# Optimization experiments

Hardware: AMD Instinct MI355X
Metric: run time of the kernel (lower is better)

## Reference

```python
import jax, jax.numpy as jnp
import numpy as np

L = 880      # flattened RootMLP param count: (1*8+8) + (8*96+96)
HID = 8      # MLP hidden width
OUT = 96     # 2*data_size
DS = 48      # data_size
T = 64       # sequence length
BATCH = 4


def setup_inputs() -> dict:
    key = jax.random.key(0)
    k1, k2, k3, k4, k5 = jax.random.split(key, 5)
    xs = jax.random.normal(k1, (BATCH, T, DS), jnp.float32)
    ts = jax.random.uniform(k2, (BATCH, T), dtype=jnp.float32)
    theta0 = 0.1 * jax.random.normal(k3, (L,), jnp.float32)
    # near-identity A so matrix powers up to A^(T-1) stay bounded
    A = 0.99 * jnp.eye(L, dtype=jnp.float32) + (0.01 / np.sqrt(L)) * jax.random.normal(k4, (L, L), jnp.float32)
    B = 0.01 * jax.random.normal(k5, (L, DS), jnp.float32)
    return {"xs": xs, "ts": ts, "theta0": theta0, "A": A, "B": B, "aux": 0}


def _forward(xs, ts, theta0, A, B):
    Bt, T_, _ = xs.shape
    I = jnp.eye(L, dtype=A.dtype)

    # A_pows[t] = A^t for t = 0..T-1, via a cumulative matmul scan
    def step(P, _):
        return P @ A, P
    _, pows = jax.lax.scan(step, I, None, length=T_)  # (T, L, L)

    # K_conv = [B, A^0(A-I)B, ..., A^(T-3)(A-I)B]  -> (T-1, L, DS)
    M = (A - I) @ B
    K_tail = jnp.einsum('tij,jd->tid', pows[:T_ - 2], M)
    K_conv = jnp.concatenate([B[None], K_tail], axis=0)

    # FFT circular convolution of input signal with K_conv over time
    u = xs[:, 1:, :]                      # (B, T-1, DS)
    u_f = jnp.fft.fft(u, axis=1)
    K_f = jnp.fft.fft(K_conv, axis=0)     # (T-1, L, DS)
    thetas = jnp.fft.ifft(jnp.einsum('tld,btd->btl', K_f, u_f), axis=1).real

    # initial-condition convolution with K_conv0 = A^tau, tau = 0..T-2
    K0 = pows[:T_ - 1]                    # (T-1, L, L)
    sig = jnp.zeros((Bt, T_ - 1, L), xs.dtype)
    sig = sig.at[:, 0, :].set(theta0)
    sig = sig.at[:, 1, :].set(-(xs[:, 0, :] @ B.T))
    sig_f = jnp.fft.fft(sig, axis=1)
    K0_f = jnp.fft.fft(K0, axis=0)
    phi0 = jnp.fft.ifft(jnp.einsum('tlm,btm->btl', K0_f, sig_f), axis=1).real

    thetas = thetas + phi0
    thetas = jnp.concatenate([jnp.broadcast_to(theta0, (Bt, 1, L)), thetas], axis=1)  # (B, T, L)

    # apply RootMLP (1 -> HID -> OUT) with params unflattened from thetas
    W0 = thetas[..., :HID]                                    # (B,T,HID): W0 is (HID,1)
    b0 = thetas[..., HID:2 * HID]
    W1 = thetas[..., 2 * HID:2 * HID + OUT * HID].reshape(Bt, T_, OUT, HID)
    b1 = thetas[..., 2 * HID + OUT * HID:]
    h = jax.nn.relu(W0 * ts[..., None] + b0)                  # (B,T,HID)
    out = jnp.einsum('btoh,bth->bto', W1, h) + b1             # (B,T,OUT)
    # reconstruction head: tanh means, softplus stds
    return jnp.concatenate([jnp.tanh(out[..., :DS]), jax.nn.softplus(out[..., DS:])], axis=-1)


def reference(xs, ts, theta0, A, B, aux):
    return _forward(xs, ts, theta0, A, B)
```

## Files before the change

### kernel.cpp

```cpp
#include <hip/hip_runtime.h>
#include <math.h>

typedef unsigned int uint;
typedef unsigned short ushort;
typedef short s16x8 __attribute__((ext_vector_type(8)));
typedef float f32x4 __attribute__((ext_vector_type(4)));
typedef uint u32x4 __attribute__((ext_vector_type(4)));

#define L     880
#define LP    896
#define NC    64
#define WS    (NC * LP)
#define DS    48
#define OUTD  96
#define KCV   3072
#define NZ    3

#define OFF_E    0
#define OFF_WF   4415488
#define OFF_WB   (OFF_WF + 63 * WS)
#define OFF_KDT  (OFF_WB + 63 * WS / 2)
#define OFF_U    (OFF_KDT + LP * KCV / 2)
#define OFF_PART (OFF_U + 256 * KCV / 2)

__device__ inline ushort f2b(float f) {
  uint u = __builtin_bit_cast(uint, f);
  u += 0x7fffu + ((u >> 16) & 1u);
  return (ushort)(u >> 16);
}
__device__ inline float b2f(ushort b) {
  uint u = ((uint)b) << 16;
  return __builtin_bit_cast(float, u);
}

__global__ __launch_bounds__(256) void k_prepE(const float* __restrict__ A,
                                               ushort* __restrict__ EN,
                                               ushort* __restrict__ ET) {
  __shared__ float T[64][65];
  const int bi = blockIdx.y * 64, bj = blockIdx.x * 64;
  const int tid = threadIdx.x;
  const int r = tid >> 2, c0 = (tid & 3) * 16;
  const int gi = bi + r;
#pragma unroll
  for (int q = 0; q < 4; ++q) {
    int c = c0 + q * 4, gj = bj + c;
    float4 v = {0.f, 0.f, 0.f, 0.f};
    if (gi < L && gj < L) {
      v = *(const float4*)(A + gi * L + gj);
      if (gi == gj)     v.x -= 0.99f;
      if (gi == gj + 1) v.y -= 0.99f;
      if (gi == gj + 2) v.z -= 0.99f;
      if (gi == gj + 3) v.w -= 0.99f;
    }
    T[r][c] = v.x; T[r][c + 1] = v.y; T[r][c + 2] = v.z; T[r][c + 3] = v.w;
  }
  __syncthreads();
  {
    union { ushort s[16]; u32x4 v[2]; } pk;
#pragma unroll
    for (int i = 0; i < 16; ++i) pk.s[i] = f2b(T[r][c0 + i]);
    *(u32x4*)(EN + (size_t)(bi + r) * LP + bj + c0)     = pk.v[0];
    *(u32x4*)(EN + (size_t)(bi + r) * LP + bj + c0 + 8) = pk.v[1];
  }
  {
    union { ushort s[16]; u32x4 v[2]; } pk;
#pragma unroll
    for (int i = 0; i < 16; ++i) pk.s[i] = f2b(T[c0 + i][r]);
    *(u32x4*)(ET + (size_t)(bj + r) * LP + bi + c0)     = pk.v[0];
    *(u32x4*)(ET + (size_t)(bj + r) * LP + bi + c0 + 8) = pk.v[1];
  }
}

__global__ void k_prepW0(const float* __restrict__ B, const float* __restrict__ th0,
                         const float* __restrict__ xs, float* __restrict__ WF,
                         ushort* __restrict__ WB) {
  int idx = blockIdx.x * 256 + threadIdx.x;
  int c = idx / LP, l = idx % LP;
  float v = 0.f;
  if (l < L) {
    if (c < DS) v = B[l * DS + c];
    else if (c == DS) v = th0[l];
    else if (c < 53) {
      int b = c - 49;
      float s = 0.f;
      for (int d = 0; d < DS; ++d) s += B[l * DS + d] * xs[(b * 64) * DS + d];
      v = -s;
    }
  }
  WF[idx] = v;
  WB[idx] = f2b(v);
}

__global__ __launch_bounds__(256) void k_ladder(
    const ushort* __restrict__ sqA, const ushort* __restrict__ sqBT, float cs2,
    ushort* __restrict__ sqOutN, ushort* __restrict__ sqOutT, int ySq,
    const ushort* __restrict__ chA, const ushort* __restrict__ chBT, float csc,
    const float* __restrict__ chWFin, float* __restrict__ chWFout,
    ushort* __restrict__ chWBout) {
  __shared__ __align__(16) ushort As[2][64][72];
  __shared__ __align__(16) ushort Bs[2][64][72];
  const int tid = threadIdx.x;
  const bool isSq = (int)blockIdx.y < ySq;
  const int n0 = blockIdx.x * 64;
  const int m0 = isSq ? blockIdx.y * 64 : ((int)blockIdx.y - ySq) * 64;
  const ushort* Ab = isSq ? sqA : chA;
  const ushort* Bb = isSq ? sqBT : chBT;
  const int r = tid >> 2, kq = (tid & 3) * 16;
  const ushort* aptr = Ab + (size_t)(m0 + r) * LP + kq;
  const ushort* bptr = Bb + (size_t)(n0 + r) * LP + kq;
  const int wv = tid >> 6, lane = tid & 63;
  const int wm = (wv >> 1) * 32, wn = (wv & 1) * 32;
  const int lr = lane & 15, lg = lane >> 4;
  f32x4 acc[2][2] = {};
  u32x4 ra0 = *(const u32x4*)aptr;
  u32x4 ra1 = *(const u32x4*)(aptr + 8);
  u32x4 rb0 = *(const u32x4*)bptr;
  u32x4 rb1 = *(const u32x4*)(bptr + 8);
  const int kI = LP / 64;
  for (int it = 0; it < kI; ++it) {
    const int cur = it & 1;
    *(u32x4*)&As[cur][r][kq]     = ra0;
    *(u32x4*)&As[cur][r][kq + 8] = ra1;
    *(u32x4*)&Bs[cur][r][kq]     = rb0;
    *(u32x4*)&Bs[cur][r][kq + 8] = rb1;
    __syncthreads();
    if (it + 1 < kI) {
      ra0 = *(const u32x4*)(aptr + (it + 1) * 64);
      ra1 = *(const u32x4*)(aptr + (it + 1) * 64 + 8);
      rb0 = *(const u32x4*)(bptr + (it + 1) * 64);
      rb1 = *(const u32x4*)(bptr + (it + 1) * 64 + 8);
    }
#pragma unroll
    for (int ks = 0; ks < 2; ++ks) {
      s16x8 a0 = *(const s16x8*)&As[cur][wm + lr][ks * 32 + lg * 8];
      s16x8 a1 = *(const s16x8*)&As[cur][wm + 16 + lr][ks * 32 + lg * 8];
      s16x8 b0 = *(const s16x8*)&Bs[cur][wn + lr][ks * 32 + lg * 8];
      s16x8 b1 = *(const s16x8*)&Bs[cur][wn + 16 + lr][ks * 32 + lg * 8];
      acc[0][0] = __builtin_amdgcn_mfma_f32_16x16x32_bf16(a0, b0, acc[0][0], 0, 0, 0);
      acc[0][1] = __builtin_amdgcn_mfma_f32_16x16x32_bf16(a0, b1, acc[0][1], 0, 0, 0);
      acc[1][0] = __builtin_amdgcn_mfma_f32_16x16x32_bf16(a1, b0, acc[1][0], 0, 0, 0);
      acc[1][1] = __builtin_amdgcn_mfma_f32_16x16x32_bf16(a1, b1, acc[1][1], 0, 0, 0);
    }
  }
  if (isSq) {
    ushort (*T)[72] = As[0];
    __syncthreads();
#pragma unroll
    for (int fm = 0; fm < 2; ++fm)
#pragma unroll
      for (int fn = 0; fn < 2; ++fn)
#pragma unroll
        for (int rr = 0; rr < 4; ++rr) {
          int mi = wm + fm * 16 + lg * 4 + rr;
          int ni = wn + fn * 16 + lr;
          float v = acc[fm][fn][rr] + cs2 * b2f(sqA[(size_t)(m0 + mi) * LP + n0 + ni]);
          ushort bv = f2b(v);
          sqOutN[(size_t)(m0 + mi) * LP + n0 + ni] = bv;
          T[ni][mi] = bv;
        }
    if (sqOutT) {
      __syncthreads();
      int rt = tid >> 2, ct0 = (tid & 3) * 16;
      u32x4 o0 = *(const u32x4*)&T[rt][ct0];
      u32x4 o1 = *(const u32x4*)&T[rt][ct0 + 8];
      *(u32x4*)(sqOutT + (size_t)(n0 + rt) * LP + m0 + ct0)     = o0;
      *(u32x4*)(sqOutT + (size_t)(n0 + rt) * LP + m0 + ct0 + 8) = o1;
    }
  } else {
#pragma unroll
    for (int fm = 0; fm < 2; ++fm)
#pragma unroll
      for (int fn = 0; fn < 2; ++fn)
#pragma unroll
        for (int rr = 0; rr < 4; ++rr) {
          int m = m0 + wm + fm * 16 + lg * 4 + rr;
          int n = n0 + wn + fn * 16 + lr;
          float v = acc[fm][fn][rr] + csc * chWFin[(size_t)m * LP + n];
          chWFout[(size_t)m * LP + n] = v;
          chWBout[(size_t)m * LP + n] = f2b(v);
        }
  }
}

__global__ void k_kd(const float* __restrict__ WF, ushort* __restrict__ KDT) {
  __shared__ float D[48][65];
  const int j = blockIdx.x;
  const int l0 = blockIdx.y * 64;
  if (j < 63) {
    const float* Wj = WF + (size_t)j * WS;
    for (int e = threadIdx.x; e < 48 * 64; e += 256) {
      int d = e >> 6, ll = e & 63;
      float v = Wj[d * LP + l0 + ll];
      if (j > 0) v -= Wj[-(int)WS + d * LP + l0 + ll];
      D[d][ll] = v;
    }
  } else {
    for (int e = threadIdx.x; e < 48 * 64; e += 256) { int d = e >> 6, ll = e & 63; D[d][ll] = 0.f; }
  }
  __syncthreads();
  for (int e = threadIdx.x; e < 48 * 64; e += 256) {
    int ll = e / 48, d = e - ll * 48;
    KDT[(size_t)(l0 + ll) * KCV + j * 48 + d] = f2b(D[d][ll]);
  }
}

__global__ void k_u(const float* __restrict__ xs, ushort* __restrict__ U) {
  int idx = (blockIdx.x * 256 + threadIdx.x) * 4;
  int rr = idx / KCV, k = idx - rr * KCV;
  ushort4 v = {0, 0, 0, 0};
  if (rr < 252 && k < 3024) {
    int b = rr / 63, tau = rr - b * 63;
    int j = k / DS, d = k - j * DS;
    int s = tau - j; if (s < 0) s += 63;
    float4 x4 = *(const float4*)(xs + (size_t)(b * 64 + s + 1) * DS + d);
    v.x = f2b(x4.x); v.y = f2b(x4.y); v.z = f2b(x4.z); v.w = f2b(x4.w);
  }
  *(ushort4*)(U + idx) = v;
}

__global__ __launch_bounds__(256) void k_conv(const ushort* __restrict__ U,
                                              const ushort* __restrict__ KDT,
                                              float* __restrict__ part) {
  __shared__ __align__(16) ushort As[2][64][72];
  __shared__ __align__(16) ushort Bs[2][64][72];
  const int tid = threadIdx.x;
  const int n0 = blockIdx.x * 64, m0 = blockIdx.y * 64;
  const int kbase = blockIdx.z * (KCV / NZ);
  const int r = tid >> 2, kq = (tid & 3) * 16;
  const ushort* aptr = U + (size_t)(m0 + r) * KCV + kbase + kq;
  const ushort* bptr = KDT + (size_t)(n0 + r) * KCV + kbase + kq;
  const int wv = tid >> 6, lane = tid & 63;
  const int wm = (wv >> 1) * 32, wn = (wv & 1) * 32;
  const int lr = lane & 15, lg = lane >> 4;
  f32x4 acc[2][2] = {};
  u32x4 ra0 = *(const u32x4*)aptr;
  u32x4 ra1 = *(const u32x4*)(aptr + 8);
  u32x4 rb0 = *(const u32x4*)bptr;
  u32x4 rb1 = *(const u32x4*)(bptr + 8);
  const int kI = (KCV / NZ) / 64;
  for (int it = 0; it < kI; ++it) {
    const int cur = it & 1;
    *(u32x4*)&As[cur][r][kq]     = ra0;
    *(u32x4*)&As[cur][r][kq + 8] = ra1;
    *(u32x4*)&Bs[cur][r][kq]     = rb0;
    *(u32x4*)&Bs[cur][r][kq + 8] = rb1;
    __syncthreads();
    if (it + 1 < kI) {
      ra0 = *(const u32x4*)(aptr + (it + 1) * 64);
      ra1 = *(const u32x4*)(aptr + (it + 1) * 64 + 8);
      rb0 = *(const u32x4*)(bptr + (it + 1) * 64);
      rb1 = *(const u32x4*)(bptr + (it + 1) * 64 + 8);
    }
#pragma unroll
    for (int ks = 0; ks < 2; ++ks) {
      s16x8 a0 = *(const s16x8*)&As[cur][wm + lr][ks * 32 + lg * 8];
      s16x8 a1 = *(const s16x8*)&As[cur][wm + 16 + lr][ks * 32 + lg * 8];
      s16x8 b0 = *(const s16x8*)&Bs[cur][wn + lr][ks * 32 + lg * 8];
      s16x8 b1 = *(const s16x8*)&Bs[cur][wn + 16 + lr][ks * 32 + lg * 8];
      acc[0][0] = __builtin_amdgcn_mfma_f32_16x16x32_bf16(a0, b0, acc[0][0], 0, 0, 0);
      acc[0][1] = __builtin_amdgcn_mfma_f32_16x16x32_bf16(a0, b1, acc[0][1], 0, 0, 0);
      acc[1][0] = __builtin_amdgcn_mfma_f32_16x16x32_bf16(a1, b0, acc[1][0], 0, 0, 0);
      acc[1][1] = __builtin_amdgcn_mfma_f32_16x16x32_bf16(a1, b1, acc[1][1], 0, 0, 0);
    }
  }
  float* pp = part + (size_t)blockIdx.z * (256 * LP);
#pragma unroll
  for (int fm = 0; fm < 2; ++fm)
#pragma unroll
    for (int fn = 0; fn < 2; ++fn)
#pragma unroll
      for (int rr = 0; rr < 4; ++rr) {
        int m = m0 + wm + fm * 16 + lg * 4 + rr;
        int n = n0 + wn + fn * 16 + lr;
        pp[(size_t)m * LP + n] = acc[fm][fn][rr];
      }
}

__global__ __launch_bounds__(256) void k_final(const float* __restrict__ part,
                                               const float* __restrict__ WF,
                                               const float* __restrict__ th0,
                                               const float* __restrict__ ts,
                                               float* __restrict__ out) {
  __shared__ float th[LP];
  const int bt = blockIdx.x, b = bt >> 6, t = bt & 63;
  for (int l = threadIdx.x; l < LP; l += 256) {
    float v = 0.f;
    if (l < L) {
      if (t == 0) v = th0[l];
      else {
        int rr = b * 63 + (t - 1);
        v = part[(size_t)rr * LP + l]
          + part[(size_t)(256 * LP) + rr * LP + l]
          + part[(size_t)(2 * 256 * LP) + rr * LP + l];
        int tau = t - 1;
        v += WF[(size_t)tau * WS + DS * LP + l];
        int tw = (tau + 62) % 63;
        v += WF[(size_t)tw * WS + (49 + b) * LP + l];
      }
    }
    th[l] = v;
  }
  __syncthreads();
  int o = threadIdx.x;
  if (o < OUTD) {
    float tv = ts[bt];
    float acc = th[784 + o];
#pragma unroll
    for (int i = 0; i < 8; ++i) {
      float h = fmaxf(th[i] * tv + th[8 + i], 0.f);
      acc += th[16 + o * 8 + i] * h;
    }
    float rs;
    if (o < DS) rs = tanhf(acc);
    else        rs = fmaxf(acc, 0.f) + log1pf(expf(-fabsf(acc)));
    out[bt * OUTD + o] = rs;
  }
}

extern "C" void kernel_launch(void* const* d_in, const int* in_sizes, int n_in,
                              void* d_out, int out_size, void* d_ws, size_t ws_size,
                              hipStream_t stream) {
  const float* xs  = (const float*)d_in[0];
  const float* ts  = (const float*)d_in[1];
  const float* th0 = (const float*)d_in[2];
  const float* A   = (const float*)d_in[3];
  const float* B   = (const float*)d_in[4];
  float* out = (float*)d_out;
  float* ws  = (float*)d_ws;

  ushort* EP   = (ushort*)(ws + OFF_E);
  const size_t PL = (size_t)LP * LP;
  ushort* EN1  = EP + 0 * PL;
  ushort* ET1  = EP + 1 * PL;
  ushort* EN2  = EP + 2 * PL;
  ushort* ET2  = EP + 3 * PL;
  ushort* EN4  = EP + 4 * PL;
  ushort* ET4  = EP + 5 * PL;
  ushort* EN8  = EP + 6 * PL;
  ushort* ET8  = EP + 7 * PL;
  ushort* EN16 = EP + 8 * PL;
  ushort* ET16 = EP + 9 * PL;
  ushort* EN32 = EP + 10 * PL;
  float*  WF   = ws + OFF_WF;
  ushort* WB   = (ushort*)(ws + OFF_WB);
  ushort* KDT  = (ushort*)(ws + OFF_KDT);
  ushort* U    = (ushort*)(ws + OFF_U);
  float*  part = ws + OFF_PART;

  const float c1 = 0.99f;
  const float c2 = c1 * c1, c4 = c2 * c2, c8 = c4 * c4, c16 = c8 * c8, c32 = c16 * c16;

  k_prepE<<<dim3(14, 14), 256, 0, stream>>>(A, EN1, ET1);
  k_prepW0<<<(NC * LP) / 256, 256, 0, stream>>>(B, th0, xs, WF, WB);
  k_u<<<(256 * KCV / 4) / 256, 256, 0, stream>>>(xs, U);

  k_ladder<<<dim3(14, 15), 256, 0, stream>>>(EN1, ET1, 2.f * c1, EN2, ET2, 14,
                                             WB, EN1, c1, WF, WF + 1 * WS, WB + (size_t)1 * WS);
  k_ladder<<<dim3(14, 16), 256, 0, stream>>>(EN2, ET2, 2.f * c2, EN4, ET4, 14,
                                             WB, EN2, c2, WF, WF + 2 * WS, WB + (size_t)2 * WS);
  k_ladder<<<dim3(14, 18), 256, 0, stream>>>(EN4, ET4, 2.f * c4, EN8, ET8, 14,
                                             WB, EN4, c4, WF, WF + 4 * WS, WB + (size_t)4 * WS);
  k_ladder<<<dim3(14, 22), 256, 0, stream>>>(EN8, ET8, 2.f * c8, EN16, ET16, 14,
                                             WB, EN8, c8, WF, WF + 8 * WS, WB + (size_t)8 * WS);
  k_ladder<<<dim3(14, 30), 256, 0, stream>>>(EN16, ET16, 2.f * c16, EN32, nullptr, 14,
                                             WB, EN16, c16, WF, WF + 16 * WS, WB + (size_t)16 * WS);
  k_ladder<<<dim3(14, 31), 256, 0, stream>>>(nullptr, nullptr, 0.f, nullptr, nullptr, 0,
                                             WB, EN32, c32, WF, WF + 32 * WS, WB + (size_t)32 * WS);

  k_kd<<<dim3(64, 14), 256, 0, stream>>>(WF, KDT);
  k_conv<<<dim3(14, 4, NZ), 256, 0, stream>>>(U, KDT, part);
  k_final<<<256, 256, 0, stream>>>(part, WF, th0, ts, out);
}
```

Measured before the change: 110.7 us.

## Enlarge GEMM tiles to 128x64, merge prep kernels, share a GEMM core macro

Three setup kernels (E transpose/convert, W0 init, U Toeplitz build) are merged into one launch that dispatches on block index. The ladder and convolution GEMMs move from 64x64 to 128x64 tiles through a shared macro, so each wave computes 4x2 MFMA fragments, giving more reuse per LDS load and fewer blocks. Chain rows are clamped to a valid-row count with guarded stores, and the WF/WB buffers grow to 64 slots to absorb the larger tiles. The cost is fewer blocks per launch (lower occupancy on a wide GPU) and more registers and LDS per block.

Measured after the change: 157.9 us. +42.6%, slower.

```diff
diff --git a/kernel.cpp b/kernel.cpp
--- a/kernel.cpp
+++ b/kernel.cpp
@@ -18,8 +18,8 @@
 
 #define OFF_E    0
 #define OFF_WF   4415488
-#define OFF_WB   (OFF_WF + 63 * WS)
-#define OFF_KDT  (OFF_WB + 63 * WS / 2)
+#define OFF_WB   (OFF_WF + 64 * WS)
+#define OFF_KDT  (OFF_WB + 64 * WS / 2)
 #define OFF_U    (OFF_KDT + LP * KCV / 2)
 #define OFF_PART (OFF_U + 256 * KCV / 2)
 
@@ -33,120 +33,159 @@
   return __builtin_bit_cast(float, u);
 }
 
-__global__ __launch_bounds__(256) void k_prepE(const float* __restrict__ A,
-                                               ushort* __restrict__ EN,
-                                               ushort* __restrict__ ET) {
-  __shared__ float T[64][65];
-  const int bi = blockIdx.y * 64, bj = blockIdx.x * 64;
+__global__ __launch_bounds__(256) void k_prep(const float* __restrict__ A,
+                                              const float* __restrict__ B,
+                                              const float* __restrict__ th0,
+                                              const float* __restrict__ xs,
+                                              ushort* __restrict__ EN,
+                                              ushort* __restrict__ ET,
+                                              float* __restrict__ WF,
+                                              ushort* __restrict__ WB,
+                                              ushort* __restrict__ U) {
+  const int blk = blockIdx.x;
   const int tid = threadIdx.x;
-  const int r = tid >> 2, c0 = (tid & 3) * 16;
-  const int gi = bi + r;
-#pragma unroll
-  for (int q = 0; q < 4; ++q) {
-    int c = c0 + q * 4, gj = bj + c;
-    float4 v = {0.f, 0.f, 0.f, 0.f};
-    if (gi < L && gj < L) {
-      v = *(const float4*)(A + gi * L + gj);
+  if (blk < 196) {
+    __shared__ float T[64][65];
+    const int bi = (blk / 14) * 64, bj = (blk % 14) * 64;
+    const int r = tid >> 2, c0 = (tid & 3) * 16;
+    const int gi = bi + r;
+#pragma unroll
+    for (int q = 0; q < 4; ++q) {
+      int c = c0 + q * 4, gj = bj + c;
+      float4 v = {0.f, 0.f, 0.f, 0.f};
+      if (gi < L && gj + 3 < L) {
+        v = *(const float4*)(A + (size_t)gi * L + gj);
+      } else if (gi < L) {
+        if (gj + 0 < L) v.x = A[(size_t)gi * L + gj];
+        if (gj + 1 < L) v.y = A[(size_t)gi * L + gj + 1];
+        if (gj + 2 < L) v.z = A[(size_t)gi * L + gj + 2];
+        if (gj + 3 < L) v.w = A[(size_t)gi * L + gj + 3];
+      }
       if (gi == gj)     v.x -= 0.99f;
       if (gi == gj + 1) v.y -= 0.99f;
       if (gi == gj + 2) v.z -= 0.99f;
       if (gi == gj + 3) v.w -= 0.99f;
-    }
-    T[r][c] = v.x; T[r][c + 1] = v.y; T[r][c + 2] = v.z; T[r][c + 3] = v.w;
-  }
-  __syncthreads();
-  {
-    union { ushort s[16]; u32x4 v[2]; } pk;
-#pragma unroll
-    for (int i = 0; i < 16; ++i) pk.s[i] = f2b(T[r][c0 + i]);
-    *(u32x4*)(EN + (size_t)(bi + r) * LP + bj + c0)     = pk.v[0];
-    *(u32x4*)(EN + (size_t)(bi + r) * LP + bj + c0 + 8) = pk.v[1];
-  }
-  {
-    union { ushort s[16]; u32x4 v[2]; } pk;
-#pragma unroll
-    for (int i = 0; i < 16; ++i) pk.s[i] = f2b(T[c0 + i][r]);
-    *(u32x4*)(ET + (size_t)(bj + r) * LP + bi + c0)     = pk.v[0];
-    *(u32x4*)(ET + (size_t)(bj + r) * LP + bi + c0 + 8) = pk.v[1];
-  }
-}
-
-__global__ void k_prepW0(const float* __restrict__ B, const float* __restrict__ th0,
-                         const float* __restrict__ xs, float* __restrict__ WF,
-                         ushort* __restrict__ WB) {
-  int idx = blockIdx.x * 256 + threadIdx.x;
-  int c = idx / LP, l = idx % LP;
-  float v = 0.f;
-  if (l < L) {
-    if (c < DS) v = B[l * DS + c];
-    else if (c == DS) v = th0[l];
-    else if (c < 53) {
-      int b = c - 49;
-      float s = 0.f;
-      for (int d = 0; d < DS; ++d) s += B[l * DS + d] * xs[(b * 64) * DS + d];
-      v = -s;
-    }
-  }
-  WF[idx] = v;
-  WB[idx] = f2b(v);
-}
+      T[r][c] = v.x; T[r][c + 1] = v.y; T[r][c + 2] = v.z; T[r][c + 3] = v.w;
+    }
+    __syncthreads();
+    {
+      union { ushort s[16]; u32x4 v[2]; } pk;
+#pragma unroll
+      for (int i = 0; i < 16; ++i) pk.s[i] = f2b(T[r][c0 + i]);
+      *(u32x4*)(EN + (size_t)(bi + r) * LP + bj + c0)     = pk.v[0];
+      *(u32x4*)(EN + (size_t)(bi + r) * LP + bj + c0 + 8) = pk.v[1];
+    }
+    {
+      union { ushort s[16]; u32x4 v[2]; } pk;
+#pragma unroll
+      for (int i = 0; i < 16; ++i) pk.s[i] = f2b(T[c0 + i][r]);
+      *(u32x4*)(ET + (size_t)(bj + r) * LP + bi + c0)     = pk.v[0];
+      *(u32x4*)(ET + (size_t)(bj + r) * LP + bi + c0 + 8) = pk.v[1];
+    }
+  } else if (blk < 420) {
+    int idx = (blk - 196) * 256 + tid;
+    int c = idx / LP, l = idx % LP;
+    float v = 0.f;
+    if (l < L) {
+      if (c < DS) v = B[l * DS + c];
+      else if (c == DS) v = th0[l];
+      else if (c < 53) {
+        int b = c - 49;
+        float s = 0.f;
+        for (int d = 0; d < DS; ++d) s += B[l * DS + d] * xs[(b * 64) * DS + d];
+        v = -s;
+      }
+    }
+    WF[idx] = v;
+    WB[idx] = f2b(v);
+  } else {
+    int idx = ((blk - 420) * 256 + tid) * 4;
+    int rr = idx / KCV, k = idx - rr * KCV;
+    ushort4 v = {0, 0, 0, 0};
+    if (rr < 252 && k < 3024) {
+      int b = rr / 63, tau = rr - b * 63;
+      int j = k / DS, d = k - j * DS;
+      int s = tau - j; if (s < 0) s += 63;
+      float4 x4 = *(const float4*)(xs + (size_t)(b * 64 + s + 1) * DS + d);
+      v.x = f2b(x4.x); v.y = f2b(x4.y); v.z = f2b(x4.z); v.w = f2b(x4.w);
+    }
+    *(ushort4*)(U + idx) = v;
+  }
+}
+
+#define LAD_ITERS (LP / 64)
+
+#define GEMM_CORE(Aop, BopT, Kdim, kIters, kOff, Mv, m0, n0)                       \
+  const int ar = tid >> 3;                                                         \
+  const int ak = (tid & 7) * 8;                                                    \
+  const int br = tid >> 2;                                                         \
+  const int bk = (tid & 3) * 8;                                                    \
+  const ushort* ap[4];                                                             \
+  _Pragma("unroll")                                                                \
+  for (int i = 0; i < 4; ++i) {                                                    \
+    int rowi = m0 + ar + i * 32;                                                   \
+    if (rowi > Mv - 1) rowi = Mv - 1;                                              \
+    ap[i] = Aop + (size_t)rowi * Kdim + kOff + ak;                                 \
+  }                                                                                \
+  const ushort* bp0 = BopT + (size_t)(n0 + br) * Kdim + kOff + bk;                 \
+  const ushort* bp1 = bp0 + 32;                                                    \
+  const int wv = tid >> 6, lane = tid & 63;                                        \
+  const int wm = (wv >> 1) * 64, wn = (wv & 1) * 32;                               \
+  const int lr = lane & 15, lg = lane >> 4;                                        \
+  f32x4 acc[4][2] = {};                                                            \
+  u32x4 ra[4], rb[2];                                                              \
+  _Pragma("unroll")                                                                \
+  for (int i = 0; i < 4; ++i) ra[i] = *(const u32x4*)ap[i];                        \
+  rb[0] = *(const u32x4*)bp0;                                                      \
+  rb[1] = *(const u32x4*)bp1;                                                      \
+  for (int it = 0; it < kIters; ++it) {                                            \
+    const int cur = it & 1;                                                        \
+    _Pragma("unroll")                                                              \
+    for (int i = 0; i < 4; ++i) *(u32x4*)&As[cur][ar + i * 32][ak] = ra[i];        \
+    *(u32x4*)&Bs[cur][br][bk]      = rb[0];                                        \
+    *(u32x4*)&Bs[cur][br][bk + 32] = rb[1];                                        \
+    __syncthreads();                                                               \
+    if (it + 1 < kIters) {                                                         \
+      _Pragma("unroll")                                                            \
+      for (int i = 0; i < 4; ++i) ra[i] = *(const u32x4*)(ap[i] + (it + 1) * 64);  \
+      rb[0] = *(const u32x4*)(bp0 + (it + 1) * 64);                                \
+      rb[1] = *(const u32x4*)(bp1 + (it + 1) * 64);                                \
+    }                                                                              \
+    _Pragma("unroll")                                                              \
+    for (int k2 = 0; k2 < 2; ++k2) {                                               \
+      s16x8 af[4], bf[2];                                                          \
+      _Pragma("unroll")                                                            \
+      for (int m = 0; m < 4; ++m) af[m] = *(const s16x8*)&As[cur][wm + m * 16 + lr][k2 * 32 + lg * 8]; \
+      _Pragma("unroll")                                                            \
+      for (int n = 0; n < 2; ++n) bf[n] = *(const s16x8*)&Bs[cur][wn + n * 16 + lr][k2 * 32 + lg * 8]; \
+      _Pragma("unroll")                                                            \
+      for (int m = 0; m < 4; ++m)                                                  \
+        _Pragma("unroll")                                                          \
+        for (int n = 0; n < 2; ++n)                                                \
+          acc[m][n] = __builtin_amdgcn_mfma_f32_16x16x32_bf16(af[m], bf[n], acc[m][n], 0, 0, 0); \
+    }                                                                              \
+  }
 
 __global__ __launch_bounds__(256) void k_ladder(
     const ushort* __restrict__ sqA, const ushort* __restrict__ sqBT, float cs2,
     ushort* __restrict__ sqOutN, ushort* __restrict__ sqOutT, int ySq,
     const ushort* __restrict__ chA, const ushort* __restrict__ chBT, float csc,
     const float* __restrict__ chWFin, float* __restrict__ chWFout,
-    ushort* __restrict__ chWBout) {
-  __shared__ __align__(16) ushort As[2][64][72];
+    ushort* __restrict__ chWBout, int Mv) {
+  __shared__ __align__(16) ushort As[2][128][72];
   __shared__ __align__(16) ushort Bs[2][64][72];
   const int tid = threadIdx.x;
   const bool isSq = (int)blockIdx.y < ySq;
   const int n0 = blockIdx.x * 64;
-  const int m0 = isSq ? blockIdx.y * 64 : ((int)blockIdx.y - ySq) * 64;
+  const int m0 = isSq ? blockIdx.y * 128 : ((int)blockIdx.y - ySq) * 128;
+  const int MvEff = isSq ? LP : Mv;
   const ushort* Ab = isSq ? sqA : chA;
   const ushort* Bb = isSq ? sqBT : chBT;
-  const int r = tid >> 2, kq = (tid & 3) * 16;
-  const ushort* aptr = Ab + (size_t)(m0 + r) * LP + kq;
-  const ushort* bptr = Bb + (size_t)(n0 + r) * LP + kq;
-  const int wv = tid >> 6, lane = tid & 63;
-  const int wm = (wv >> 1) * 32, wn = (wv & 1) * 32;
-  const int lr = lane & 15, lg = lane >> 4;
-  f32x4 acc[2][2] = {};
-  u32x4 ra0 = *(const u32x4*)aptr;
-  u32x4 ra1 = *(const u32x4*)(aptr + 8);
-  u32x4 rb0 = *(const u32x4*)bptr;
-  u32x4 rb1 = *(const u32x4*)(bptr + 8);
-  const int kI = LP / 64;
-  for (int it = 0; it < kI; ++it) {
-    const int cur = it & 1;
-    *(u32x4*)&As[cur][r][kq]     = ra0;
-    *(u32x4*)&As[cur][r][kq + 8] = ra1;
-    *(u32x4*)&Bs[cur][r][kq]     = rb0;
-    *(u32x4*)&Bs[cur][r][kq + 8] = rb1;
-    __syncthreads();
-    if (it + 1 < kI) {
-      ra0 = *(const u32x4*)(aptr + (it + 1) * 64);
-      ra1 = *(const u32x4*)(aptr + (it + 1) * 64 + 8);
-      rb0 = *(const u32x4*)(bptr + (it + 1) * 64);
-      rb1 = *(const u32x4*)(bptr + (it + 1) * 64 + 8);
-    }
-#pragma unroll
-    for (int ks = 0; ks < 2; ++ks) {
-      s16x8 a0 = *(const s16x8*)&As[cur][wm + lr][ks * 32 + lg * 8];
-      s16x8 a1 = *(const s16x8*)&As[cur][wm + 16 + lr][ks * 32 + lg * 8];
-      s16x8 b0 = *(const s16x8*)&Bs[cur][wn + lr][ks * 32 + lg * 8];
-      s16x8 b1 = *(const s16x8*)&Bs[cur][wn + 16 + lr][ks * 32 + lg * 8];
-      acc[0][0] = __builtin_amdgcn_mfma_f32_16x16x32_bf16(a0, b0, acc[0][0], 0, 0, 0);
-      acc[0][1] = __builtin_amdgcn_mfma_f32_16x16x32_bf16(a0, b1, acc[0][1], 0, 0, 0);
-      acc[1][0] = __builtin_amdgcn_mfma_f32_16x16x32_bf16(a1, b0, acc[1][0], 0, 0, 0);
-      acc[1][1] = __builtin_amdgcn_mfma_f32_16x16x32_bf16(a1, b1, acc[1][1], 0, 0, 0);
-    }
-  }
+  GEMM_CORE(Ab, Bb, LP, LAD_ITERS, 0, MvEff, m0, n0)
   if (isSq) {
-    ushort (*T)[72] = As[0];
-    __syncthreads();
-#pragma unroll
-    for (int fm = 0; fm < 2; ++fm)
+    ushort* T = &As[0][0][0];
+#pragma unroll
+    for (int fm = 0; fm < 4; ++fm)
 #pragma unroll
       for (int fn = 0; fn < 2; ++fn)
 #pragma unroll
@@ -156,36 +195,63 @@
           float v = acc[fm][fn][rr] + cs2 * b2f(sqA[(size_t)(m0 + mi) * LP + n0 + ni]);
           ushort bv = f2b(v);
           sqOutN[(size_t)(m0 + mi) * LP + n0 + ni] = bv;
-          T[ni][mi] = bv;
+          T[ni * 136 + mi] = bv;
         }
     if (sqOutT) {
       __syncthreads();
-      int rt = tid >> 2, ct0 = (tid & 3) * 16;
-      u32x4 o0 = *(const u32x4*)&T[rt][ct0];
-      u32x4 o1 = *(const u32x4*)&T[rt][ct0 + 8];
-      *(u32x4*)(sqOutT + (size_t)(n0 + rt) * LP + m0 + ct0)     = o0;
-      *(u32x4*)(sqOutT + (size_t)(n0 + rt) * LP + m0 + ct0 + 8) = o1;
+      const int nr = tid >> 2, seg = (tid & 3) * 32;
+#pragma unroll
+      for (int q = 0; q < 4; ++q) {
+        u32x4 o = *(const u32x4*)&T[nr * 136 + seg + q * 8];
+        *(u32x4*)(sqOutT + (size_t)(n0 + nr) * LP + m0 + seg + q * 8) = o;
+      }
     }
   } else {
 #pragma unroll
-    for (int fm = 0; fm < 2; ++fm)
+    for (int fm = 0; fm < 4; ++fm)
 #pragma unroll
       for (int fn = 0; fn < 2; ++fn)
 #pragma unroll
         for (int rr = 0; rr < 4; ++rr) {
-          int m = m0 + wm + fm * 16 + lg * 4 + rr;
-          int n = n0 + wn + fn * 16 + lr;
-          float v = acc[fm][fn][rr] + csc * chWFin[(size_t)m * LP + n];
-          chWFout[(size_t)m * LP + n] = v;
-          chWBout[(size_t)m * LP + n] = f2b(v);
+          int mi = wm + fm * 16 + lg * 4 + rr;
+          int m = m0 + mi;
+          if (m < Mv) {
+            int n = n0 + wn + fn * 16 + lr;
+            float v = acc[fm][fn][rr] + csc * chWFin[(size_t)m * LP + n];
+            chWFout[(size_t)m * LP + n] = v;
+            chWBout[(size_t)m * LP + n] = f2b(v);
+          }
         }
   }
+}
+
+__global__ __launch_bounds__(256) void k_conv(const ushort* __restrict__ U,
+                                              const ushort* __restrict__ KDT,
+                                              float* __restrict__ part) {
+  __shared__ __align__(16) ushort As[2][128][72];
+  __shared__ __align__(16) ushort Bs[2][64][72];
+  const int tid = threadIdx.x;
+  const int n0 = blockIdx.x * 64;
+  const int m0 = blockIdx.y * 128;
+  const int kOff = blockIdx.z * (KCV / NZ);
+  GEMM_CORE(U, KDT, KCV, (KCV / NZ) / 64, kOff, 256, m0, n0)
+  float* pp = part + (size_t)blockIdx.z * (256 * LP);
+#pragma unroll
+  for (int fm = 0; fm < 4; ++fm)
+#pragma unroll
+    for (int fn = 0; fn < 2; ++fn)
+#pragma unroll
+      for (int rr = 0; rr < 4; ++rr) {
+        int m = m0 + wm + fm * 16 + lg * 4 + rr;
+        int n = n0 + wn + fn * 16 + lr;
+        pp[(size_t)m * LP + n] = acc[fm][fn][rr];
+      }
 }
 
 __global__ void k_kd(const float* __restrict__ WF, ushort* __restrict__ KDT) {
   __shared__ float D[48][65];
-  const int j = blockIdx.x;
-  const int l0 = blockIdx.y * 64;
+  const int j = blockIdx.y;
+  const int l0 = blockIdx.x * 64;
   if (j < 63) {
     const float* Wj = WF + (size_t)j * WS;
     for (int e = threadIdx.x; e < 48 * 64; e += 256) {
@@ -202,78 +268,6 @@
     int ll = e / 48, d = e - ll * 48;
     KDT[(size_t)(l0 + ll) * KCV + j * 48 + d] = f2b(D[d][ll]);
   }
-}
-
-__global__ void k_u(const float* __restrict__ xs, ushort* __restrict__ U) {
-  int idx = (blockIdx.x * 256 + threadIdx.x) * 4;
-  int rr = idx / KCV, k = idx - rr * KCV;
-  ushort4 v = {0, 0, 0, 0};
-  if (rr < 252 && k < 3024) {
-    int b = rr / 63, tau = rr - b * 63;
-    int j = k / DS, d = k - j * DS;
-    int s = tau - j; if (s < 0) s += 63;
-    float4 x4 = *(const float4*)(xs + (size_t)(b * 64 + s + 1) * DS + d);
-    v.x = f2b(x4.x); v.y = f2b(x4.y); v.z = f2b(x4.z); v.w = f2b(x4.w);
-  }
-  *(ushort4*)(U + idx) = v;
-}
-
-__global__ __launch_bounds__(256) void k_conv(const ushort* __restrict__ U,
-                                              const ushort* __restrict__ KDT,
-                                              float* __restrict__ part) {
-  __shared__ __align__(16) ushort As[2][64][72];
-  __shared__ __align__(16) ushort Bs[2][64][72];
-  const int tid = threadIdx.x;
-  const int n0 = blockIdx.x * 64, m0 = blockIdx.y * 64;
-  const int kbase = blockIdx.z * (KCV / NZ);
-  const int r = tid >> 2, kq = (tid & 3) * 16;
-  const ushort* aptr = U + (size_t)(m0 + r) * KCV + kbase + kq;
-  const ushort* bptr = KDT + (size_t)(n0 + r) * KCV + kbase + kq;
-  const int wv = tid >> 6, lane = tid & 63;
-  const int wm = (wv >> 1) * 32, wn = (wv & 1) * 32;
-  const int lr = lane & 15, lg = lane >> 4;
-  f32x4 acc[2][2] = {};
-  u32x4 ra0 = *(const u32x4*)aptr;
-  u32x4 ra1 = *(const u32x4*)(aptr + 8);
-  u32x4 rb0 = *(const u32x4*)bptr;
-  u32x4 rb1 = *(const u32x4*)(bptr + 8);
-  const int kI = (KCV / NZ) / 64;
-  for (int it = 0; it < kI; ++it) {
-    const int cur = it & 1;
-    *(u32x4*)&As[cur][r][kq]     = ra0;
-    *(u32x4*)&As[cur][r][kq + 8] = ra1;
-    *(u32x4*)&Bs[cur][r][kq]     = rb0;
-    *(u32x4*)&Bs[cur][r][kq + 8] = rb1;
-    __syncthreads();
-    if (it + 1 < kI) {
-      ra0 = *(const u32x4*)(aptr + (it + 1) * 64);
-      ra1 = *(const u32x4*)(aptr + (it + 1) * 64 + 8);
-      rb0 = *(const u32x4*)(bptr + (it + 1) * 64);
-      rb1 = *(const u32x4*)(bptr + (it + 1) * 64 + 8);
-    }
-#pragma unroll
-    for (int ks = 0; ks < 2; ++ks) {
-      s16x8 a0 = *(const s16x8*)&As[cur][wm + lr][ks * 32 + lg * 8];
-      s16x8 a1 = *(const s16x8*)&As[cur][wm + 16 + lr][ks * 32 + lg * 8];
-      s16x8 b0 = *(const s16x8*)&Bs[cur][wn + lr][ks * 32 + lg * 8];
-      s16x8 b1 = *(const s16x8*)&Bs[cur][wn + 16 + lr][ks * 32 + lg * 8];
-      acc[0][0] = __builtin_amdgcn_mfma_f32_16x16x32_bf16(a0, b0, acc[0][0], 0, 0, 0);
-      acc[0][1] = __builtin_amdgcn_mfma_f32_16x16x32_bf16(a0, b1, acc[0][1], 0, 0, 0);
-      acc[1][0] = __builtin_amdgcn_mfma_f32_16x16x32_bf16(a1, b0, acc[1][0], 0, 0, 0);
-      acc[1][1] = __builtin_amdgcn_mfma_f32_16x16x32_bf16(a1, b1, acc[1][1], 0, 0, 0);
-    }
-  }
-  float* pp = part + (size_t)blockIdx.z * (256 * LP);
-#pragma unroll
-  for (int fm = 0; fm < 2; ++fm)
-#pragma unroll
-    for (int fn = 0; fn < 2; ++fn)
-#pragma unroll
-      for (int rr = 0; rr < 4; ++rr) {
-        int m = m0 + wm + fm * 16 + lg * 4 + rr;
-        int n = n0 + wn + fn * 16 + lr;
-        pp[(size_t)m * LP + n] = acc[fm][fn][rr];
-      }
 }
 
 __global__ __launch_bounds__(256) void k_final(const float* __restrict__ part,
@@ -350,24 +344,22 @@
   const float c1 = 0.99f;
   const float c2 = c1 * c1, c4 = c2 * c2, c8 = c4 * c4, c16 = c8 * c8, c32 = c16 * c16;
 
-  k_prepE<<<dim3(14, 14), 256, 0, stream>>>(A, EN1, ET1);
-  k_prepW0<<<(NC * LP) / 256, 256, 0, stream>>>(B, th0, xs, WF, WB);
-  k_u<<<(256 * KCV / 4) / 256, 256, 0, stream>>>(xs, U);
-
-  k_ladder<<<dim3(14, 15), 256, 0, stream>>>(EN1, ET1, 2.f * c1, EN2, ET2, 14,
-                                             WB, EN1, c1, WF, WF + 1 * WS, WB + (size_t)1 * WS);
-  k_ladder<<<dim3(14, 16), 256, 0, stream>>>(EN2, ET2, 2.f * c2, EN4, ET4, 14,
-                                             WB, EN2, c2, WF, WF + 2 * WS, WB + (size_t)2 * WS);
-  k_ladder<<<dim3(14, 18), 256, 0, stream>>>(EN4, ET4, 2.f * c4, EN8, ET8, 14,
-                                             WB, EN4, c4, WF, WF + 4 * WS, WB + (size_t)4 * WS);
-  k_ladder<<<dim3(14, 22), 256, 0, stream>>>(EN8, ET8, 2.f * c8, EN16, ET16, 14,
-                                             WB, EN8, c8, WF, WF + 8 * WS, WB + (size_t)8 * WS);
-  k_ladder<<<dim3(14, 30), 256, 0, stream>>>(EN16, ET16, 2.f * c16, EN32, nullptr, 14,
-                                             WB, EN16, c16, WF, WF + 16 * WS, WB + (size_t)16 * WS);
-  k_ladder<<<dim3(14, 31), 256, 0, stream>>>(nullptr, nullptr, 0.f, nullptr, nullptr, 0,
-                                             WB, EN32, c32, WF, WF + 32 * WS, WB + (size_t)32 * WS);
-
-  k_kd<<<dim3(64, 14), 256, 0, stream>>>(WF, KDT);
-  k_conv<<<dim3(14, 4, NZ), 256, 0, stream>>>(U, KDT, part);
+  k_prep<<<1188, 256, 0, stream>>>(A, B, th0, xs, EN1, ET1, WF, WB, U);
+
+  k_ladder<<<dim3(14, 8), 256, 0, stream>>>(EN1, ET1, 2.f * c1, EN2, ET2, 7,
+                                            WB, EN1, c1, WF, WF + 1 * WS, WB + (size_t)1 * WS, 64);
+  k_ladder<<<dim3(14, 8), 256, 0, stream>>>(EN2, ET2, 2.f * c2, EN4, ET4, 7,
+                                            WB, EN2, c2, WF, WF + 2 * WS, WB + (size_t)2 * WS, 128);
+  k_ladder<<<dim3(14, 9), 256, 0, stream>>>(EN4, ET4, 2.f * c4, EN8, ET8, 7,
+                                            WB, EN4, c4, WF, WF + 4 * WS, WB + (size_t)4 * WS, 256);
+  k_ladder<<<dim3(14, 11), 256, 0, stream>>>(EN8, ET8, 2.f * c8, EN16, ET16, 7,
+                                             WB, EN8, c8, WF, WF + 8 * WS, WB + (size_t)8 * WS, 512);
+  k_ladder<<<dim3(14, 15), 256, 0, stream>>>(EN16, ET16, 2.f * c16, EN32, nullptr, 7,
+                                             WB, EN16, c16, WF, WF + 16 * WS, WB + (size_t)16 * WS, 1024);
+  k_ladder<<<dim3(14, 16), 256, 0, stream>>>(nullptr, nullptr, 0.f, nullptr, nullptr, 0,
+                                             WB, EN32, c32, WF, WF + 32 * WS, WB + (size_t)32 * WS, 2048);
+
+  k_kd<<<dim3(14, 64), 256, 0, stream>>>(WF, KDT);
+  k_conv<<<dim3(14, 2, NZ), 256, 0, stream>>>(U, KDT, part);
   k_final<<<256, 256, 0, stream>>>(part, WF, th0, ts, out);
 }
```
